# Kernel tuning notes

Measured on AMD Instinct MI355X. Metric: run time of the kernel, lower is better.

The kernel has to match this reference:

```python
import jax, jax.numpy as jnp
import numpy as np

N = 50000
E = 800000
NODE_F = 128
HID = 96
TEMP_F = 10


def setup_inputs() -> dict:
    key = jax.random.key(0)
    ks = jax.random.split(key, 10)
    x = jax.random.normal(ks[0], (N, NODE_F), dtype=jnp.float32)
    edge_index = jax.random.randint(ks[1], (2, E), 0, N, dtype=jnp.int64)
    temporal = jax.random.normal(ks[2], (N, TEMP_F), dtype=jnp.float32)
    # GCNConv: lin weight [in, out] (no bias in lin), separate bias [out]
    W_gcn = jax.random.normal(ks[3], (NODE_F, HID), dtype=jnp.float32) / np.sqrt(NODE_F)
    b_gcn = jnp.zeros((HID,), dtype=jnp.float32)
    W1 = jax.random.normal(ks[4], (HID + TEMP_F, HID), dtype=jnp.float32) / np.sqrt(HID + TEMP_F)
    b1 = jax.random.normal(ks[5], (HID,), dtype=jnp.float32) * 0.01
    W2 = jax.random.normal(ks[6], (HID + NODE_F, 1), dtype=jnp.float32) / np.sqrt(HID + NODE_F)
    b2 = jax.random.normal(ks[7], (1,), dtype=jnp.float32) * 0.01
    return {"x": x, "edge_index": edge_index, "temporal": temporal,
            "W_gcn": W_gcn, "b_gcn": b_gcn, "W1": W1, "b1": b1, "W2": W2, "b2": b2}


def _gcn_conv(x, edge_index, W, b):
    n = x.shape[0]
    loop = jnp.arange(n, dtype=edge_index.dtype)
    src = jnp.concatenate([edge_index[0], loop])  # [E+N]
    dst = jnp.concatenate([edge_index[1], loop])
    # symmetric normalization with self-loops (PyG gcn_norm)
    ones = jnp.ones(src.shape[0], dtype=x.dtype)
    deg = jax.ops.segment_sum(ones, dst, num_segments=n)
    dinv = jnp.where(deg > 0, jax.lax.rsqrt(deg), 0.0)
    norm = dinv[src] * dinv[dst]  # [E+N]
    h = x @ W  # [N, HID]
    msg = h[src] * norm[:, None]  # [E+N, HID] gather + scale
    out = jax.ops.segment_sum(msg, dst, num_segments=n)  # scatter-add
    return out + b


def reference(x, edge_index, temporal, W_gcn, b_gcn, W1, b1, W2, b2):
    h = jax.nn.relu(_gcn_conv(x, edge_index, W_gcn, b_gcn))  # [N, HID]
    h = jnp.concatenate([h, temporal], axis=-1)              # [N, HID+TEMP_F]
    h = jax.nn.relu(h @ W1 + b1)                             # [N, HID]
    h = jnp.concatenate([h, x], axis=-1)                     # [N, HID+NODE_F]
    return jax.nn.relu(h @ W2 + b2)                          # [N, 1]
```

## Files before the change

### kernel.cpp

```cpp
#include <hip/hip_runtime.h>
#include <hip/hip_bf16.h>

#define NN 50000
#define NPAD 50048
#define NE 800000
#define NF 128
#define HH 96
#define TF 10
#define Z1DIM (HH + TF)
#define ZK 128
#define NCH 4
#define CW 24
#define NBK 196
#define CAP 5120
#define EPB 8192

typedef __attribute__((ext_vector_type(8))) short short8;
typedef __attribute__((ext_vector_type(8))) unsigned short ushort8;
typedef __attribute__((ext_vector_type(4))) float f32x4;

__device__ __forceinline__ float bu2f(unsigned short u) {
    union { unsigned int i; float f; } c;
    c.i = ((unsigned int)u) << 16;
    return c.f;
}
__device__ __forceinline__ unsigned short f2bu(float f) {
    union { __hip_bfloat16 h; unsigned short u; } c;
    c.h = __float2bfloat16(f);
    return c.u;
}

__global__ void k_init(int* __restrict__ bcur, int* __restrict__ off) {
    int t = threadIdx.x;
    if (t < NBK) bcur[t] = t * CAP;
    if (t == 255) off[NN] = NE;
}

__global__ __launch_bounds__(256) void k_fillA(const int* __restrict__ ei,
                                               int* __restrict__ bcur,
                                               int* __restrict__ temp) {
    __shared__ int hist[NBK], base[NBK];
    const int t = threadIdx.x;
    for (int m = t; m < NBK; m += 256) hist[m] = 0;
    __syncthreads();
    const int e0 = blockIdx.x * EPB;
    const int ecap = min(e0 + EPB, NE);
    for (int e = e0 + t; e < ecap; e += 256) {
        int d = ei[NE + e];
        atomicAdd(&hist[d >> 8], 1);
    }
    __syncthreads();
    for (int m = t; m < NBK; m += 256) {
        int c = hist[m];
        base[m] = c ? atomicAdd(&bcur[m], c) : 0;
        hist[m] = 0;
    }
    __syncthreads();
    for (int e = e0 + t; e < ecap; e += 256) {
        int d = ei[NE + e], s = ei[e];
        int b = d >> 8;
        int r = atomicAdd(&hist[b], 1);
        temp[base[b] + r] = ((d & 255) << 16) | s;
    }
}

__global__ __launch_bounds__(256) void k_fillB(const int* __restrict__ temp,
                                               const int* __restrict__ bcur,
                                               unsigned short* __restrict__ csr,
                                               int* __restrict__ off) {
    __shared__ int ls[256], lc[256];
    const int b = blockIdx.x, t = threadIdx.x;
    int szt = (t < NBK) ? (bcur[t] - t * CAP) : 0;
    ls[t] = szt;
    __syncthreads();
#pragma unroll
    for (int d = 1; d < 256; d <<= 1) {
        int u = (t >= d) ? ls[t - d] : 0;
        __syncthreads();
        ls[t] += u;
        __syncthreads();
    }
    const int g0 = (b > 0) ? ls[b - 1] : 0;
    __syncthreads();
    ls[t] = 0;
    __syncthreads();
    const int seg0 = b * CAP;
    const int m = bcur[b] - seg0;
    for (int k = t; k < m; k += 256) atomicAdd(&ls[temp[seg0 + k] >> 16], 1);
    __syncthreads();
    const int myc = ls[t];
    lc[t] = myc;
    __syncthreads();
#pragma unroll
    for (int d = 1; d < 256; d <<= 1) {
        int u = (t >= d) ? lc[t - d] : 0;
        __syncthreads();
        lc[t] += u;
        __syncthreads();
    }
    const int myoff = lc[t] - myc;
    __syncthreads();
    lc[t] = myoff;
    const int i = b * 256 + t;
    if (i < NN) off[i] = g0 + myoff;
    __syncthreads();
    for (int k = t; k < m; k += 256) {
        int v = temp[seg0 + k];
        int r = atomicAdd(&lc[v >> 16], 1);
        csr[g0 + r] = (unsigned short)(v & 0xFFFF);
    }
}

#define WBLK (NF * HH / 4 / 256)
#define W1BLK (HH * ZK / 4 / 256)
#define ZTBLK (NPAD / 32)
#define ZPBLK 5
__global__ void k_prep(const float* __restrict__ W,
                       const float* __restrict__ W1, const float* __restrict__ tmp,
                       unsigned short* __restrict__ Wt,
                       unsigned short* __restrict__ Wt1, unsigned short* __restrict__ zb) {
    int b = blockIdx.x;
    if (b < WBLK) {
        int e = (b * 256 + threadIdx.x) * 4;
        int n = e >> 7, k = e & 127;
        ushort4 v;
        v.x = f2bu(W[(k + 0) * HH + n]);
        v.y = f2bu(W[(k + 1) * HH + n]);
        v.z = f2bu(W[(k + 2) * HH + n]);
        v.w = f2bu(W[(k + 3) * HH + n]);
        *(ushort4*)(Wt + e) = v;
    } else if (b < WBLK + W1BLK) {
        int e = ((b - WBLK) * 256 + threadIdx.x) * 4;
        int n = e >> 7, k = e & 127;
        ushort4 v;
        v.x = (k + 0 < Z1DIM) ? f2bu(W1[(k + 0) * HH + n]) : (unsigned short)0;
        v.y = (k + 1 < Z1DIM) ? f2bu(W1[(k + 1) * HH + n]) : (unsigned short)0;
        v.z = (k + 2 < Z1DIM) ? f2bu(W1[(k + 2) * HH + n]) : (unsigned short)0;
        v.w = (k + 3 < Z1DIM) ? f2bu(W1[(k + 3) * HH + n]) : (unsigned short)0;
        *(ushort4*)(Wt1 + e) = v;
    } else if (b < WBLK + W1BLK + ZTBLK) {
        int t4 = ((b - WBLK - W1BLK) * 256 + threadIdx.x) * 4;
        int i = t4 >> 5, cc = t4 & 31;
        ushort4 v; v.x = v.y = v.z = v.w = 0;
        if (i < NN) {
            if (cc + 0 < TF) v.x = f2bu(tmp[(size_t)i * TF + cc + 0]);
            if (cc + 1 < TF) v.y = f2bu(tmp[(size_t)i * TF + cc + 1]);
            if (cc + 2 < TF) v.z = f2bu(tmp[(size_t)i * TF + cc + 2]);
            if (cc + 3 < TF) v.w = f2bu(tmp[(size_t)i * TF + cc + 3]);
        }
        *(ushort4*)(zb + (size_t)i * ZK + HH + cc) = v;
    } else {
        int t4 = ((b - WBLK - W1BLK - ZTBLK) * 256 + threadIdx.x) * 4;
        if (t4 < (NPAD - NN) * HH) {
            int i = NN + t4 / HH, j = t4 % HH;
            ushort4 z; z.x = z.y = z.z = z.w = 0;
            *(ushort4*)(zb + (size_t)i * ZK + j) = z;
        }
    }
}

__global__ __launch_bounds__(256) void k_gemm(const float* __restrict__ x,
                                              const unsigned short* __restrict__ Wt,
                                              const int* __restrict__ off,
                                              const float* __restrict__ W2,
                                              unsigned short* __restrict__ hp_c,
                                              float* __restrict__ xw2) {
    const int wave = threadIdx.x >> 6;
    const int lane = threadIdx.x & 63;
    const int quad = lane >> 4;
    const int l16 = lane & 15;
    const int Mbase = blockIdx.x * 64 + wave * 16;
    const int row = Mbase + l16;
    const bool valid = row < NN;

    const float* xr = x + (size_t)row * NF + quad * 8;
    const unsigned short* brow = Wt + (size_t)l16 * NF + quad * 8;

    f32x4 acc[6] = {};
    float xs = 0.f;
#pragma unroll
    for (int ks = 0; ks < 4; ++ks) {
        short8 a = {};
        if (valid) {
            float4 f0 = *(const float4*)(xr + ks * 32);
            float4 f1 = *(const float4*)(xr + ks * 32 + 4);
            const float4 w0 = *(const float4*)(W2 + HH + quad * 8 + ks * 32);
            const float4 w1 = *(const float4*)(W2 + HH + quad * 8 + ks * 32 + 4);
            xs = fmaf(f0.x, w0.x, xs); xs = fmaf(f0.y, w0.y, xs);
            xs = fmaf(f0.z, w0.z, xs); xs = fmaf(f0.w, w0.w, xs);
            xs = fmaf(f1.x, w1.x, xs); xs = fmaf(f1.y, w1.y, xs);
            xs = fmaf(f1.z, w1.z, xs); xs = fmaf(f1.w, w1.w, xs);
            a[0] = (short)f2bu(f0.x); a[1] = (short)f2bu(f0.y);
            a[2] = (short)f2bu(f0.z); a[3] = (short)f2bu(f0.w);
            a[4] = (short)f2bu(f1.x); a[5] = (short)f2bu(f1.y);
            a[6] = (short)f2bu(f1.z); a[7] = (short)f2bu(f1.w);
        }
#pragma unroll
        for (int nt = 0; nt < 6; ++nt) {
            short8 bfrag = *(const short8*)(brow + (size_t)nt * 16 * NF + ks * 32);
            acc[nt] = __builtin_amdgcn_mfma_f32_16x16x32_bf16(a, bfrag, acc[nt], 0, 0, 0);
        }
    }
    xs += __shfl_xor(xs, 16, 64);
    xs += __shfl_xor(xs, 32, 64);
    if (quad == 0 && valid) xw2[row] = xs;

    const int r0 = Mbase + quad * 4;
    float dv[4];
#pragma unroll
    for (int k = 0; k < 4; ++k) {
        int r = r0 + k;
        dv[k] = (r < NN) ? rsqrtf((float)(off[r + 1] - off[r]) + 1.f) : 0.f;
    }
#pragma unroll
    for (int nt = 0; nt < 6; ++nt) {
        int n = nt * 16 + l16;
        int c = n / CW, jj = n - c * CW;
        unsigned short* dst = hp_c + (size_t)c * NN * CW + jj;
#pragma unroll
        for (int k = 0; k < 4; ++k)
            if (r0 + k < NN) dst[(size_t)(r0 + k) * CW] = f2bu(acc[nt][k] * dv[k]);
    }
}

#define RPC2 1172
#define AGGB (4 * RPC2)
__global__ __launch_bounds__(256) void k_agg(const unsigned short* __restrict__ hp_c,
                                             const int* __restrict__ off,
                                             const unsigned short* __restrict__ csr,
                                             const float* __restrict__ bg,
                                             unsigned short* __restrict__ zb) {
    const int b = blockIdx.x;
    const int slot = b & 7;
    const int c = slot >> 1;
    const int r = (b >> 3) * 2 + (slot & 1);
    const int item = r * 256 + threadIdx.x;
    if (item >= NN * 6) return;
    const int i = item / 6;
    const int sub = item - i * 6;
    const int q = sub >> 1;
    const int h = sub & 1;
    const unsigned short* base = hp_c + (size_t)c * NN * CW + q * 8;

    float a0, a1, a2, a3, a4, a5, a6, a7;
    if (h == 0) {
        ushort8 sv = *(const ushort8*)(base + (size_t)i * CW);
        a0 = bu2f(sv[0]); a1 = bu2f(sv[1]); a2 = bu2f(sv[2]); a3 = bu2f(sv[3]);
        a4 = bu2f(sv[4]); a5 = bu2f(sv[5]); a6 = bu2f(sv[6]); a7 = bu2f(sv[7]);
    } else {
        a0 = a1 = a2 = a3 = a4 = a5 = a6 = a7 = 0.f;
    }

    const int start = off[i];
    const int end = off[i + 1];
    const float dv = rsqrtf((float)(end - start) + 1.f);
    int k = start + h;
    for (; k + 6 < end; k += 8) {
        int s0 = csr[k], s1 = csr[k + 2], s2 = csr[k + 4], s3 = csr[k + 6];
        ushort8 v0 = *(const ushort8*)(base + (size_t)s0 * CW);
        ushort8 v1 = *(const ushort8*)(base + (size_t)s1 * CW);
        ushort8 v2 = *(const ushort8*)(base + (size_t)s2 * CW);
        ushort8 v3 = *(const ushort8*)(base + (size_t)s3 * CW);
        a0 += (bu2f(v0[0]) + bu2f(v1[0])) + (bu2f(v2[0]) + bu2f(v3[0]));
        a1 += (bu2f(v0[1]) + bu2f(v1[1])) + (bu2f(v2[1]) + bu2f(v3[1]));
        a2 += (bu2f(v0[2]) + bu2f(v1[2])) + (bu2f(v2[2]) + bu2f(v3[2]));
        a3 += (bu2f(v0[3]) + bu2f(v1[3])) + (bu2f(v2[3]) + bu2f(v3[3]));
        a4 += (bu2f(v0[4]) + bu2f(v1[4])) + (bu2f(v2[4]) + bu2f(v3[4]));
        a5 += (bu2f(v0[5]) + bu2f(v1[5])) + (bu2f(v2[5]) + bu2f(v3[5]));
        a6 += (bu2f(v0[6]) + bu2f(v1[6])) + (bu2f(v2[6]) + bu2f(v3[6]));
        a7 += (bu2f(v0[7]) + bu2f(v1[7])) + (bu2f(v2[7]) + bu2f(v3[7]));
    }
    for (; k < end; k += 2) {
        ushort8 v0 = *(const ushort8*)(base + (size_t)csr[k] * CW);
        a0 += bu2f(v0[0]); a1 += bu2f(v0[1]); a2 += bu2f(v0[2]); a3 += bu2f(v0[3]);
        a4 += bu2f(v0[4]); a5 += bu2f(v0[5]); a6 += bu2f(v0[6]); a7 += bu2f(v0[7]);
    }
    a0 += __shfl_xor(a0, 1, 64); a1 += __shfl_xor(a1, 1, 64);
    a2 += __shfl_xor(a2, 1, 64); a3 += __shfl_xor(a3, 1, 64);
    a4 += __shfl_xor(a4, 1, 64); a5 += __shfl_xor(a5, 1, 64);
    a6 += __shfl_xor(a6, 1, 64); a7 += __shfl_xor(a7, 1, 64);
    if (h == 0) {
        const int j = c * CW + q * 8;
        ushort8 o;
        o[0] = f2bu(fmaxf(fmaf(dv, a0, bg[j + 0]), 0.f));
        o[1] = f2bu(fmaxf(fmaf(dv, a1, bg[j + 1]), 0.f));
        o[2] = f2bu(fmaxf(fmaf(dv, a2, bg[j + 2]), 0.f));
        o[3] = f2bu(fmaxf(fmaf(dv, a3, bg[j + 3]), 0.f));
        o[4] = f2bu(fmaxf(fmaf(dv, a4, bg[j + 4]), 0.f));
        o[5] = f2bu(fmaxf(fmaf(dv, a5, bg[j + 5]), 0.f));
        o[6] = f2bu(fmaxf(fmaf(dv, a6, bg[j + 6]), 0.f));
        o[7] = f2bu(fmaxf(fmaf(dv, a7, bg[j + 7]), 0.f));
        *(ushort8*)(zb + (size_t)i * ZK + j) = o;
    }
}

__global__ __launch_bounds__(256) void k_mlp2(const unsigned short* __restrict__ zb,
                                              const unsigned short* __restrict__ Wt1,
                                              const float* __restrict__ b1,
                                              const float* __restrict__ W2,
                                              const float* __restrict__ b2,
                                              const float* __restrict__ xw2,
                                              float* __restrict__ out) {
    const int wave = threadIdx.x >> 6;
    const int lane = threadIdx.x & 63;
    const int quad = lane >> 4;
    const int l16 = lane & 15;
    const int Mbase = blockIdx.x * 64 + wave * 16;

    const unsigned short* arow = zb + (size_t)(Mbase + l16) * ZK + quad * 8;
    const unsigned short* brow = Wt1 + (size_t)l16 * ZK + quad * 8;

    f32x4 acc[6] = {};
#pragma unroll
    for (int ks = 0; ks < 4; ++ks) {
        short8 a = *(const short8*)(arow + ks * 32);
#pragma unroll
        for (int nt = 0; nt < 6; ++nt) {
            short8 bfrag = *(const short8*)(brow + (size_t)nt * 16 * ZK + ks * 32);
            acc[nt] = __builtin_amdgcn_mfma_f32_16x16x32_bf16(a, bfrag, acc[nt], 0, 0, 0);
        }
    }
    float bb[6], wa[6];
#pragma unroll
    for (int nt = 0; nt < 6; ++nt) {
        int c = nt * 16 + l16;
        bb[nt] = b1[c];
        wa[nt] = W2[c];
    }
    const float bias2 = b2[0];

#pragma unroll
    for (int reg = 0; reg < 4; ++reg) {
        const int r = Mbase + quad * 4 + reg;
        float p = 0.f;
#pragma unroll
        for (int nt = 0; nt < 6; ++nt)
            p = fmaf(fmaxf(acc[nt][reg] + bb[nt], 0.f), wa[nt], p);
#pragma unroll
        for (int m = 1; m < 16; m <<= 1) p += __shfl_xor(p, m, 64);
        if (l16 == 0 && r < NN) out[r] = fmaxf(p + xw2[r] + bias2, 0.f);
    }
}

extern "C" void kernel_launch(void* const* d_in, const int* in_sizes, int n_in,
                              void* d_out, int out_size, void* d_ws, size_t ws_size,
                              hipStream_t stream) {
    const float* x   = (const float*)d_in[0];
    const int*   ei  = (const int*)d_in[1];
    const float* tmp = (const float*)d_in[2];
    const float* Wg  = (const float*)d_in[3];
    const float* bg  = (const float*)d_in[4];
    const float* W1  = (const float*)d_in[5];
    const float* b1  = (const float*)d_in[6];
    const float* W2  = (const float*)d_in[7];
    const float* b2  = (const float*)d_in[8];
    float* out = (float*)d_out;

    char* base = (char*)d_ws;
    int* off  = (int*)base;
    int* bcur = off + 65536;
    unsigned short* csr = (unsigned short*)(bcur + 512);
    unsigned short* Wt  = (unsigned short*)(base + ((size_t)4 << 20));
    unsigned short* Wt1 = Wt + NF * HH;
    unsigned short* hp_c = Wt1 + HH * ZK;
    unsigned short* zb = hp_c + (size_t)NN * HH;
    float* xw2 = (float*)(zb + (size_t)NPAD * ZK);
    int* temp = (int*)zb;

    k_init <<<1, 256, 0, stream>>>(bcur, off);
    k_fillA<<<(NE + EPB - 1) / EPB, 256, 0, stream>>>(ei, bcur, temp);
    k_fillB<<<NBK, 256, 0, stream>>>(temp, bcur, csr, off);
    k_prep <<<WBLK + W1BLK + ZTBLK + ZPBLK, 256, 0, stream>>>(Wg, W1, tmp, Wt, Wt1, zb);
    k_gemm <<<NPAD / 64, 256, 0, stream>>>(x, Wt, off, W2, hp_c, xw2);
    k_agg  <<<AGGB, 256, 0, stream>>>(hp_c, off, csr, bg, zb);
    k_mlp2 <<<NPAD / 64, 256, 0, stream>>>(zb, Wt1, b1, W2, b2, xw2, out);
}
```

Baseline: 182.4 us.

## Merge CSR build with prep and GEMM kernels; widen aggregation per thread

Folds the edge-bucketing pass into the weight/temporal prep kernel, and the per-bucket CSR finalisation into the feature GEMM kernel. Seven launches become five, and independent work shares a grid. Degrees now come from a global atomic counter, so the GEMM no longer depends on CSR offsets. Aggregation now has each thread pair cover a full 24-column chunk over contiguous halves of the neighbour list, rather than 8 columns with interleaved edges. Risks are heavy global atomics on deg, higher register use per thread, and fewer aggregation threads.

```diff
diff --git a/kernel.cpp b/kernel.cpp
--- a/kernel.cpp
+++ b/kernel.cpp
@@ -13,7 +13,8 @@
 #define CW 24
 #define NBK 196
 #define CAP 5120
-#define EPB 8192
+#define EPB 4096
+#define FILLA_B ((NE + EPB - 1) / EPB)
 
 typedef __attribute__((ext_vector_type(8))) short short8;
 typedef __attribute__((ext_vector_type(8))) unsigned short ushort8;
@@ -30,98 +31,58 @@
     return c.u;
 }
 
-__global__ void k_init(int* __restrict__ bcur, int* __restrict__ off) {
-    int t = threadIdx.x;
-    if (t < NBK) bcur[t] = t * CAP;
-    if (t == 255) off[NN] = NE;
-}
-
-__global__ __launch_bounds__(256) void k_fillA(const int* __restrict__ ei,
-                                               int* __restrict__ bcur,
-                                               int* __restrict__ temp) {
-    __shared__ int hist[NBK], base[NBK];
-    const int t = threadIdx.x;
-    for (int m = t; m < NBK; m += 256) hist[m] = 0;
-    __syncthreads();
-    const int e0 = blockIdx.x * EPB;
-    const int ecap = min(e0 + EPB, NE);
-    for (int e = e0 + t; e < ecap; e += 256) {
-        int d = ei[NE + e];
-        atomicAdd(&hist[d >> 8], 1);
-    }
-    __syncthreads();
-    for (int m = t; m < NBK; m += 256) {
-        int c = hist[m];
-        base[m] = c ? atomicAdd(&bcur[m], c) : 0;
-        hist[m] = 0;
-    }
-    __syncthreads();
-    for (int e = e0 + t; e < ecap; e += 256) {
-        int d = ei[NE + e], s = ei[e];
-        int b = d >> 8;
-        int r = atomicAdd(&hist[b], 1);
-        temp[base[b] + r] = ((d & 255) << 16) | s;
-    }
-}
-
-__global__ __launch_bounds__(256) void k_fillB(const int* __restrict__ temp,
-                                               const int* __restrict__ bcur,
-                                               unsigned short* __restrict__ csr,
-                                               int* __restrict__ off) {
-    __shared__ int ls[256], lc[256];
-    const int b = blockIdx.x, t = threadIdx.x;
-    int szt = (t < NBK) ? (bcur[t] - t * CAP) : 0;
-    ls[t] = szt;
-    __syncthreads();
-#pragma unroll
-    for (int d = 1; d < 256; d <<= 1) {
-        int u = (t >= d) ? ls[t - d] : 0;
-        __syncthreads();
-        ls[t] += u;
-        __syncthreads();
-    }
-    const int g0 = (b > 0) ? ls[b - 1] : 0;
-    __syncthreads();
-    ls[t] = 0;
-    __syncthreads();
-    const int seg0 = b * CAP;
-    const int m = bcur[b] - seg0;
-    for (int k = t; k < m; k += 256) atomicAdd(&ls[temp[seg0 + k] >> 16], 1);
-    __syncthreads();
-    const int myc = ls[t];
-    lc[t] = myc;
-    __syncthreads();
-#pragma unroll
-    for (int d = 1; d < 256; d <<= 1) {
-        int u = (t >= d) ? lc[t - d] : 0;
-        __syncthreads();
-        lc[t] += u;
-        __syncthreads();
-    }
-    const int myoff = lc[t] - myc;
-    __syncthreads();
-    lc[t] = myoff;
-    const int i = b * 256 + t;
-    if (i < NN) off[i] = g0 + myoff;
-    __syncthreads();
-    for (int k = t; k < m; k += 256) {
-        int v = temp[seg0 + k];
-        int r = atomicAdd(&lc[v >> 16], 1);
-        csr[g0 + r] = (unsigned short)(v & 0xFFFF);
-    }
+__global__ void k_init(int* __restrict__ bcur, int* __restrict__ off,
+                       int* __restrict__ deg) {
+    int i = blockIdx.x * 256 + threadIdx.x;
+    if (i < NN) deg[i] = 0;
+    if (i < NBK) bcur[i] = i * CAP;
+    if (i == NN) off[NN] = NE;
 }
 
 #define WBLK (NF * HH / 4 / 256)
 #define W1BLK (HH * ZK / 4 / 256)
 #define ZTBLK (NPAD / 32)
 #define ZPBLK 5
-__global__ void k_prep(const float* __restrict__ W,
-                       const float* __restrict__ W1, const float* __restrict__ tmp,
-                       unsigned short* __restrict__ Wt,
-                       unsigned short* __restrict__ Wt1, unsigned short* __restrict__ zb) {
-    int b = blockIdx.x;
+__global__ __launch_bounds__(256) void k_pre(const int* __restrict__ ei,
+                                             int* __restrict__ bcur,
+                                             int* __restrict__ temp,
+                                             int* __restrict__ deg,
+                                             const float* __restrict__ W,
+                                             const float* __restrict__ W1,
+                                             const float* __restrict__ tmp,
+                                             unsigned short* __restrict__ Wt,
+                                             unsigned short* __restrict__ Wt1,
+                                             unsigned short* __restrict__ zb) {
+    const int t = threadIdx.x;
+    if (blockIdx.x < FILLA_B) {
+        __shared__ int hist[NBK], bas[NBK];
+        for (int m = t; m < NBK; m += 256) hist[m] = 0;
+        __syncthreads();
+        const int e0 = blockIdx.x * EPB;
+        const int ecap = min(e0 + EPB, NE);
+        for (int e = e0 + t; e < ecap; e += 256) {
+            int d = ei[NE + e];
+            atomicAdd(&hist[d >> 8], 1);
+            atomicAdd(&deg[d], 1);
+        }
+        __syncthreads();
+        for (int m = t; m < NBK; m += 256) {
+            int c = hist[m];
+            bas[m] = c ? atomicAdd(&bcur[m], c) : 0;
+            hist[m] = 0;
+        }
+        __syncthreads();
+        for (int e = e0 + t; e < ecap; e += 256) {
+            int d = ei[NE + e], s = ei[e];
+            int b = d >> 8;
+            int r = atomicAdd(&hist[b], 1);
+            temp[bas[b] + r] = ((d & 255) << 16) | s;
+        }
+        return;
+    }
+    int b = blockIdx.x - FILLA_B;
     if (b < WBLK) {
-        int e = (b * 256 + threadIdx.x) * 4;
+        int e = (b * 256 + t) * 4;
         int n = e >> 7, k = e & 127;
         ushort4 v;
         v.x = f2bu(W[(k + 0) * HH + n]);
@@ -130,7 +91,7 @@
         v.w = f2bu(W[(k + 3) * HH + n]);
         *(ushort4*)(Wt + e) = v;
     } else if (b < WBLK + W1BLK) {
-        int e = ((b - WBLK) * 256 + threadIdx.x) * 4;
+        int e = ((b - WBLK) * 256 + t) * 4;
         int n = e >> 7, k = e & 127;
         ushort4 v;
         v.x = (k + 0 < Z1DIM) ? f2bu(W1[(k + 0) * HH + n]) : (unsigned short)0;
@@ -139,7 +100,7 @@
         v.w = (k + 3 < Z1DIM) ? f2bu(W1[(k + 3) * HH + n]) : (unsigned short)0;
         *(ushort4*)(Wt1 + e) = v;
     } else if (b < WBLK + W1BLK + ZTBLK) {
-        int t4 = ((b - WBLK - W1BLK) * 256 + threadIdx.x) * 4;
+        int t4 = ((b - WBLK - W1BLK) * 256 + t) * 4;
         int i = t4 >> 5, cc = t4 & 31;
         ushort4 v; v.x = v.y = v.z = v.w = 0;
         if (i < NN) {
@@ -150,7 +111,7 @@
         }
         *(ushort4*)(zb + (size_t)i * ZK + HH + cc) = v;
     } else {
-        int t4 = ((b - WBLK - W1BLK - ZTBLK) * 256 + threadIdx.x) * 4;
+        int t4 = ((b - WBLK - W1BLK - ZTBLK) * 256 + t) * 4;
         if (t4 < (NPAD - NN) * HH) {
             int i = NN + t4 / HH, j = t4 % HH;
             ushort4 z; z.x = z.y = z.z = z.w = 0;
@@ -159,17 +120,66 @@
     }
 }
 
-__global__ __launch_bounds__(256) void k_gemm(const float* __restrict__ x,
-                                              const unsigned short* __restrict__ Wt,
-                                              const int* __restrict__ off,
-                                              const float* __restrict__ W2,
-                                              unsigned short* __restrict__ hp_c,
-                                              float* __restrict__ xw2) {
-    const int wave = threadIdx.x >> 6;
-    const int lane = threadIdx.x & 63;
+__global__ __launch_bounds__(256) void k_gg(const int* __restrict__ temp,
+                                            const int* __restrict__ bcur,
+                                            unsigned short* __restrict__ csr,
+                                            int* __restrict__ off,
+                                            const float* __restrict__ x,
+                                            const unsigned short* __restrict__ Wt,
+                                            const float* __restrict__ W2,
+                                            const int* __restrict__ deg,
+                                            unsigned short* __restrict__ hp_c,
+                                            float* __restrict__ xw2) {
+    const int t = threadIdx.x;
+    if (blockIdx.x < NBK) {
+        __shared__ int ls[256], lc[256];
+        const int b = blockIdx.x;
+        int szt = (t < NBK) ? (bcur[t] - t * CAP) : 0;
+        ls[t] = szt;
+        __syncthreads();
+#pragma unroll
+        for (int d = 1; d < 256; d <<= 1) {
+            int u = (t >= d) ? ls[t - d] : 0;
+            __syncthreads();
+            ls[t] += u;
+            __syncthreads();
+        }
+        const int g0 = (b > 0) ? ls[b - 1] : 0;
+        __syncthreads();
+        ls[t] = 0;
+        __syncthreads();
+        const int seg0 = b * CAP;
+        const int m = bcur[b] - seg0;
+        for (int k = t; k < m; k += 256) atomicAdd(&ls[temp[seg0 + k] >> 16], 1);
+        __syncthreads();
+        const int myc = ls[t];
+        lc[t] = myc;
+        __syncthreads();
+#pragma unroll
+        for (int d = 1; d < 256; d <<= 1) {
+            int u = (t >= d) ? lc[t - d] : 0;
+            __syncthreads();
+            lc[t] += u;
+            __syncthreads();
+        }
+        const int myoff = lc[t] - myc;
+        __syncthreads();
+        lc[t] = myoff;
+        const int i = b * 256 + t;
+        if (i < NN) off[i] = g0 + myoff;
+        __syncthreads();
+        for (int k = t; k < m; k += 256) {
+            int v = temp[seg0 + k];
+            int r = atomicAdd(&lc[v >> 16], 1);
+            csr[g0 + r] = (unsigned short)(v & 0xFFFF);
+        }
+        return;
+    }
+    const int wave = t >> 6;
+    const int lane = t & 63;
     const int quad = lane >> 4;
     const int l16 = lane & 15;
-    const int Mbase = blockIdx.x * 64 + wave * 16;
+    const int Mbase = (blockIdx.x - NBK) * 64 + wave * 16;
     const int row = Mbase + l16;
     const bool valid = row < NN;
 
@@ -210,7 +220,7 @@
 #pragma unroll
     for (int k = 0; k < 4; ++k) {
         int r = r0 + k;
-        dv[k] = (r < NN) ? rsqrtf((float)(off[r + 1] - off[r]) + 1.f) : 0.f;
+        dv[k] = (r < NN) ? rsqrtf((float)deg[r] + 1.f) : 0.f;
     }
 #pragma unroll
     for (int nt = 0; nt < 6; ++nt) {
@@ -223,8 +233,8 @@
     }
 }
 
-#define RPC2 1172
-#define AGGB (4 * RPC2)
+#define RPC2 196
+#define AGGB (8 * RPC2)
 __global__ __launch_bounds__(256) void k_agg(const unsigned short* __restrict__ hp_c,
                                              const int* __restrict__ off,
                                              const unsigned short* __restrict__ csr,
@@ -235,62 +245,74 @@
     const int c = slot >> 1;
     const int r = (b >> 3) * 2 + (slot & 1);
     const int item = r * 256 + threadIdx.x;
-    if (item >= NN * 6) return;
-    const int i = item / 6;
-    const int sub = item - i * 6;
-    const int q = sub >> 1;
-    const int h = sub & 1;
-    const unsigned short* base = hp_c + (size_t)c * NN * CW + q * 8;
-
-    float a0, a1, a2, a3, a4, a5, a6, a7;
+    if (item >= NN * 2) return;
+    const int i = item >> 1;
+    const int h = item & 1;
+    const unsigned short* __restrict__ base = hp_c + (size_t)c * NN * CW;
+
+    float a[CW];
     if (h == 0) {
-        ushort8 sv = *(const ushort8*)(base + (size_t)i * CW);
-        a0 = bu2f(sv[0]); a1 = bu2f(sv[1]); a2 = bu2f(sv[2]); a3 = bu2f(sv[3]);
-        a4 = bu2f(sv[4]); a5 = bu2f(sv[5]); a6 = bu2f(sv[6]); a7 = bu2f(sv[7]);
+        const unsigned short* sp = base + (size_t)i * CW;
+        ushort8 s0 = *(const ushort8*)(sp);
+        ushort8 s1 = *(const ushort8*)(sp + 8);
+        ushort8 s2 = *(const ushort8*)(sp + 16);
+#pragma unroll
+        for (int j = 0; j < 8; ++j) {
+            a[j] = bu2f(s0[j]); a[8 + j] = bu2f(s1[j]); a[16 + j] = bu2f(s2[j]);
+        }
     } else {
-        a0 = a1 = a2 = a3 = a4 = a5 = a6 = a7 = 0.f;
+#pragma unroll
+        for (int j = 0; j < CW; ++j) a[j] = 0.f;
     }
 
     const int start = off[i];
     const int end = off[i + 1];
-    const float dv = rsqrtf((float)(end - start) + 1.f);
-    int k = start + h;
-    for (; k + 6 < end; k += 8) {
-        int s0 = csr[k], s1 = csr[k + 2], s2 = csr[k + 4], s3 = csr[k + 6];
-        ushort8 v0 = *(const ushort8*)(base + (size_t)s0 * CW);
-        ushort8 v1 = *(const ushort8*)(base + (size_t)s1 * CW);
-        ushort8 v2 = *(const ushort8*)(base + (size_t)s2 * CW);
-        ushort8 v3 = *(const ushort8*)(base + (size_t)s3 * CW);
-        a0 += (bu2f(v0[0]) + bu2f(v1[0])) + (bu2f(v2[0]) + bu2f(v3[0]));
-        a1 += (bu2f(v0[1]) + bu2f(v1[1])) + (bu2f(v2[1]) + bu2f(v3[1]));
-        a2 += (bu2f(v0[2]) + bu2f(v1[2])) + (bu2f(v2[2]) + bu2f(v3[2]));
-        a3 += (bu2f(v0[3]) + bu2f(v1[3])) + (bu2f(v2[3]) + bu2f(v3[3]));
-        a4 += (bu2f(v0[4]) + bu2f(v1[4])) + (bu2f(v2[4]) + bu2f(v3[4]));
-        a5 += (bu2f(v0[5]) + bu2f(v1[5])) + (bu2f(v2[5]) + bu2f(v3[5]));
-        a6 += (bu2f(v0[6]) + bu2f(v1[6])) + (bu2f(v2[6]) + bu2f(v3[6]));
-        a7 += (bu2f(v0[7]) + bu2f(v1[7])) + (bu2f(v2[7]) + bu2f(v3[7]));
-    }
-    for (; k < end; k += 2) {
-        ushort8 v0 = *(const ushort8*)(base + (size_t)csr[k] * CW);
-        a0 += bu2f(v0[0]); a1 += bu2f(v0[1]); a2 += bu2f(v0[2]); a3 += bu2f(v0[3]);
-        a4 += bu2f(v0[4]); a5 += bu2f(v0[5]); a6 += bu2f(v0[6]); a7 += bu2f(v0[7]);
-    }
-    a0 += __shfl_xor(a0, 1, 64); a1 += __shfl_xor(a1, 1, 64);
-    a2 += __shfl_xor(a2, 1, 64); a3 += __shfl_xor(a3, 1, 64);
-    a4 += __shfl_xor(a4, 1, 64); a5 += __shfl_xor(a5, 1, 64);
-    a6 += __shfl_xor(a6, 1, 64); a7 += __shfl_xor(a7, 1, 64);
+    const int len = end - start;
+    const float dv = rsqrtf((float)len + 1.f);
+    const int half0 = (len + 1) >> 1;
+    int k = h ? start + half0 : start;
+    const int ke = h ? end : start + half0;
+    for (; k + 1 < ke; k += 2) {
+        const unsigned short* p0 = base + (size_t)csr[k] * CW;
+        const unsigned short* p1 = base + (size_t)csr[k + 1] * CW;
+        ushort8 v0 = *(const ushort8*)(p0);
+        ushort8 v1 = *(const ushort8*)(p0 + 8);
+        ushort8 v2 = *(const ushort8*)(p0 + 16);
+        ushort8 w0 = *(const ushort8*)(p1);
+        ushort8 w1 = *(const ushort8*)(p1 + 8);
+        ushort8 w2 = *(const ushort8*)(p1 + 16);
+#pragma unroll
+        for (int j = 0; j < 8; ++j) {
+            a[j]      += bu2f(v0[j]) + bu2f(w0[j]);
+            a[8 + j]  += bu2f(v1[j]) + bu2f(w1[j]);
+            a[16 + j] += bu2f(v2[j]) + bu2f(w2[j]);
+        }
+    }
+    if (k < ke) {
+        const unsigned short* p0 = base + (size_t)csr[k] * CW;
+        ushort8 v0 = *(const ushort8*)(p0);
+        ushort8 v1 = *(const ushort8*)(p0 + 8);
+        ushort8 v2 = *(const ushort8*)(p0 + 16);
+#pragma unroll
+        for (int j = 0; j < 8; ++j) {
+            a[j] += bu2f(v0[j]); a[8 + j] += bu2f(v1[j]); a[16 + j] += bu2f(v2[j]);
+        }
+    }
+#pragma unroll
+    for (int j = 0; j < CW; ++j) a[j] += __shfl_xor(a[j], 1, 64);
     if (h == 0) {
-        const int j = c * CW + q * 8;
-        ushort8 o;
-        o[0] = f2bu(fmaxf(fmaf(dv, a0, bg[j + 0]), 0.f));
-        o[1] = f2bu(fmaxf(fmaf(dv, a1, bg[j + 1]), 0.f));
-        o[2] = f2bu(fmaxf(fmaf(dv, a2, bg[j + 2]), 0.f));
-        o[3] = f2bu(fmaxf(fmaf(dv, a3, bg[j + 3]), 0.f));
-        o[4] = f2bu(fmaxf(fmaf(dv, a4, bg[j + 4]), 0.f));
-        o[5] = f2bu(fmaxf(fmaf(dv, a5, bg[j + 5]), 0.f));
-        o[6] = f2bu(fmaxf(fmaf(dv, a6, bg[j + 6]), 0.f));
-        o[7] = f2bu(fmaxf(fmaf(dv, a7, bg[j + 7]), 0.f));
-        *(ushort8*)(zb + (size_t)i * ZK + j) = o;
+        const int j0 = c * CW;
+        ushort8 o0, o1, o2;
+#pragma unroll
+        for (int j = 0; j < 8; ++j) {
+            o0[j] = f2bu(fmaxf(fmaf(dv, a[j],      bg[j0 + j]),      0.f));
+            o1[j] = f2bu(fmaxf(fmaf(dv, a[8 + j],  bg[j0 + 8 + j]),  0.f));
+            o2[j] = f2bu(fmaxf(fmaf(dv, a[16 + j], bg[j0 + 16 + j]), 0.f));
+        }
+        unsigned short* zp = zb + (size_t)i * ZK + j0;
+        *(ushort8*)(zp) = o0;
+        *(ushort8*)(zp + 8) = o1;
+        *(ushort8*)(zp + 16) = o2;
     }
 }
 
@@ -358,20 +380,20 @@
 
     char* base = (char*)d_ws;
     int* off  = (int*)base;
-    int* bcur = off + 65536;
-    unsigned short* csr = (unsigned short*)(bcur + 512);
-    unsigned short* Wt  = (unsigned short*)(base + ((size_t)4 << 20));
+    int* bcur = (int*)(base + (256 << 10));
+    int* deg  = (int*)(base + (260 << 10));
+    unsigned short* csr = (unsigned short*)(base + (512 << 10));
+    unsigned short* Wt  = (unsigned short*)(base + ((size_t)3 << 20));
     unsigned short* Wt1 = Wt + NF * HH;
-    unsigned short* hp_c = Wt1 + HH * ZK;
-    unsigned short* zb = hp_c + (size_t)NN * HH;
-    float* xw2 = (float*)(zb + (size_t)NPAD * ZK);
-    int* temp = (int*)zb;
-
-    k_init <<<1, 256, 0, stream>>>(bcur, off);
-    k_fillA<<<(NE + EPB - 1) / EPB, 256, 0, stream>>>(ei, bcur, temp);
-    k_fillB<<<NBK, 256, 0, stream>>>(temp, bcur, csr, off);
-    k_prep <<<WBLK + W1BLK + ZTBLK + ZPBLK, 256, 0, stream>>>(Wg, W1, tmp, Wt, Wt1, zb);
-    k_gemm <<<NPAD / 64, 256, 0, stream>>>(x, Wt, off, W2, hp_c, xw2);
+    unsigned short* hp_c = (unsigned short*)(base + ((size_t)4 << 20));
+    unsigned short* zb  = (unsigned short*)(base + ((size_t)14 << 20));
+    float* xw2 = (float*)(base + ((size_t)27 << 20));
+    int* temp  = (int*)(base + ((size_t)28 << 20));
+
+    k_init <<<(NN + 256) / 256, 256, 0, stream>>>(bcur, off, deg);
+    k_pre  <<<FILLA_B + WBLK + W1BLK + ZTBLK + ZPBLK, 256, 0, stream>>>(
+                ei, bcur, temp, deg, Wg, W1, tmp, Wt, Wt1, zb);
+    k_gg   <<<NBK + NPAD / 64, 256, 0, stream>>>(temp, bcur, csr, off, x, Wt, W2, deg, hp_c, xw2);
     k_agg  <<<AGGB, 256, 0, stream>>>(hp_c, off, csr, bg, zb);
     k_mlp2 <<<NPAD / 64, 256, 0, stream>>>(zb, Wt1, b1, W2, b2, xw2, out);
 }
```

Result: slower. 197.9 us (+8.5%).
